# Optimization experiments

Hardware: AMD Instinct MI355X
Metric: run time of the kernel (lower is better)

The kernel has to match this reference:

```python
import jax, jax.numpy as jnp
import numpy as np

N, F_IN, HID, H1, E = 50000, 512, 128, 4, 800000
NEG_SLOPE = 0.2

def setup_inputs() -> dict:
    key = jax.random.key(0)
    ks = jax.random.split(key, 10)
    s = lambda fan: 1.0 / np.sqrt(fan)
    x = jax.random.normal(ks[0], (N, F_IN), jnp.float32)
    edge_index = jax.random.randint(ks[1], (2, E), 0, N, jnp.int32)
    W1 = jax.random.normal(ks[2], (F_IN, H1 * HID), jnp.float32) * s(F_IN)
    a_src1 = jax.random.normal(ks[3], (H1, HID), jnp.float32) * s(HID)
    a_dst1 = jax.random.normal(ks[4], (H1, HID), jnp.float32) * s(HID)
    b1 = jnp.zeros((H1 * HID,), jnp.float32)
    W2 = jax.random.normal(ks[5], (H1 * HID, HID), jnp.float32) * s(H1 * HID)
    a_src2 = jax.random.normal(ks[6], (1, HID), jnp.float32) * s(HID)
    a_dst2 = jax.random.normal(ks[7], (1, HID), jnp.float32) * s(HID)
    b2 = jnp.zeros((HID,), jnp.float32)
    return {"x": x, "edge_index": edge_index, "W1": W1, "a_src1": a_src1,
            "a_dst1": a_dst1, "b1": b1, "W2": W2, "a_src2": a_src2,
            "a_dst2": a_dst2, "b2": b2}

def _gat(x, src, dst, W, a_src, a_dst, b, n):
    H, C = a_src.shape
    h = (x @ W).reshape(-1, H, C)                      # [N, H, C]
    # per-edge attention logits: alpha_src[src] + alpha_dst[dst]
    e = jax.nn.leaky_relu((h * a_src).sum(-1)[src] + (h * a_dst).sum(-1)[dst],
                          NEG_SLOPE)                   # [E', H]
    # segment softmax over destination node
    m = jax.ops.segment_max(e, dst, num_segments=n)
    p = jnp.exp(e - m[dst])
    denom = jax.ops.segment_sum(p, dst, num_segments=n)
    alpha = p / (denom[dst] + 1e-16)
    # weighted scatter-add aggregation
    out = jax.ops.segment_sum(h[src] * alpha[:, :, None], dst, num_segments=n)
    return out.reshape(-1, H * C) + b

def reference(x, edge_index, W1, a_src1, a_dst1, b1, W2, a_src2, a_dst2, b2):
    loops = jnp.arange(N, dtype=edge_index.dtype)      # add_self_loops=True
    src = jnp.concatenate([edge_index[0], loops])
    dst = jnp.concatenate([edge_index[1], loops])
    h = jax.nn.elu(_gat(x, src, dst, W1, a_src1, a_dst1, b1, N))
    return _gat(h, src, dst, W2, a_src2, a_dst2, b2, N)
```

## Files before the change

kernel.cpp:

```cpp
#include <hip/hip_runtime.h>
#include <hip/hip_bf16.h>
#include <math.h>

#define NEG_SLOPE 0.2f

constexpr int N_NODES = 50000;
constexpr int F_IN    = 512;
constexpr int HID     = 128;
constexpr int H1      = 4;
constexpr int E_EDGES = 800000;
constexpr int E_TOT   = E_EDGES + N_NODES;

typedef __attribute__((ext_vector_type(8))) short short8;
typedef __attribute__((ext_vector_type(4))) float floatx4;
typedef __attribute__((ext_vector_type(8))) unsigned short ushort8v;
typedef __attribute__((ext_vector_type(4))) unsigned short ushort4v;
typedef __attribute__((ext_vector_type(2))) unsigned short ushort2v;

__device__ __forceinline__ unsigned short f2bf(float f) {
  union { float f; unsigned int u; } v; v.f = f;
  unsigned int u = v.u + 0x7FFFu + ((v.u >> 16) & 1u);
  return (unsigned short)(u >> 16);
}
__device__ __forceinline__ float bf2f(unsigned short b) {
  union { unsigned int u; float f; } v; v.u = ((unsigned int)b) << 16; return v.f;
}

__device__ __forceinline__ void store_val(float* p, float v) { *p = v; }
__device__ __forceinline__ void store_val(unsigned short* p, float v) { *p = f2bf(v); }

template <int CPT>
__device__ __forceinline__ void load_cvt(const unsigned short* p, float* v) {
  if constexpr (CPT == 8) {
    ushort8v u = *(const ushort8v*)p;
#pragma unroll
    for (int c = 0; c < 8; ++c) v[c] = bf2f(u[c]);
  } else if constexpr (CPT == 4) {
    ushort4v u = *(const ushort4v*)p;
#pragma unroll
    for (int c = 0; c < 4; ++c) v[c] = bf2f(u[c]);
  } else {
    ushort2v u = *(const ushort2v*)p;
#pragma unroll
    for (int c = 0; c < 2; ++c) v[c] = bf2f(u[c]);
  }
}
template <int CPT>
__device__ __forceinline__ void load_cvt(const float* p, float* v) {
#pragma unroll
  for (int c = 0; c < CPT; c += 4) *(float4*)(v + c) = *(const float4*)(p + c);
}

template <int CPT>
__device__ __forceinline__ void store_vec(unsigned short* p, const float* v) {
  if constexpr (CPT == 8) {
    ushort8v o;
#pragma unroll
    for (int c = 0; c < 8; ++c) o[c] = f2bf(v[c]);
    *(ushort8v*)p = o;
  } else if constexpr (CPT == 4) {
    ushort4v o;
#pragma unroll
    for (int c = 0; c < 4; ++c) o[c] = f2bf(v[c]);
    *(ushort4v*)p = o;
  } else {
    ushort2v o;
#pragma unroll
    for (int c = 0; c < 2; ++c) o[c] = f2bf(v[c]);
    *(ushort2v*)p = o;
  }
}
template <int CPT>
__device__ __forceinline__ void store_vec(float* p, const float* v) {
#pragma unroll
  for (int c = 0; c < CPT; c += 4) *(float4*)(p + c) = *(const float4*)(v + c);
}

__device__ __forceinline__ void async_load16(const void* g, void* lds) {
  __builtin_amdgcn_global_load_lds(
      (const __attribute__((address_space(1))) unsigned int*)g,
      (__attribute__((address_space(3))) unsigned int*)lds, 16, 0, 0);
}

__global__ void zero_int_kernel(int* p, int n) {
  int i = blockIdx.x * blockDim.x + threadIdx.x;
  if (i < n) p[i] = 0;
}

__global__ void hist_kernel(const int* __restrict__ ei, int* __restrict__ counts) {
  int i = blockIdx.x * blockDim.x + threadIdx.x;
  if (i < E_EDGES) {
    atomicAdd(&counts[ei[E_EDGES + i]], 1);
  } else if (i < E_TOT) {
    atomicAdd(&counts[i - E_EDGES], 1);
  }
}

__global__ void scan1_kernel(const int* __restrict__ cnt, int* __restrict__ part,
                             int* __restrict__ bsum, int n) {
  __shared__ int buf[256];
  int tid = threadIdx.x, i = blockIdx.x * 256 + tid;
  int v = (i < n) ? cnt[i] : 0;
  buf[tid] = v;
  __syncthreads();
  for (int s = 1; s < 256; s <<= 1) {
    int t = (tid >= s) ? buf[tid - s] : 0;
    __syncthreads();
    buf[tid] += t;
    __syncthreads();
  }
  if (i < n) part[i] = buf[tid] - v;
  if (tid == 255) bsum[blockIdx.x] = buf[255];
}

__global__ void scan2_kernel(int* __restrict__ bsum, int nb) {
  __shared__ int buf[256];
  int tid = threadIdx.x;
  int v = (tid < nb) ? bsum[tid] : 0;
  buf[tid] = v;
  __syncthreads();
  for (int s = 1; s < 256; s <<= 1) {
    int t = (tid >= s) ? buf[tid - s] : 0;
    __syncthreads();
    buf[tid] += t;
    __syncthreads();
  }
  if (tid < nb) bsum[tid] = buf[tid] - v;
  if (tid == 255) bsum[nb] = buf[255];
}

__global__ void scan3_kernel(const int* __restrict__ part, const int* __restrict__ bsum,
                             int* __restrict__ offs, int n) {
  int i = blockIdx.x * 256 + threadIdx.x;
  if (i < n) offs[i] = part[i] + bsum[blockIdx.x];
  if (i == 0) offs[n] = bsum[(n + 255) / 256];
}

__global__ void scatter_kernel(const int* __restrict__ ei, const int* __restrict__ offs,
                               int* __restrict__ cursor, int* __restrict__ sorted_src) {
  int i = blockIdx.x * blockDim.x + threadIdx.x;
  if (i >= E_TOT) return;
  int s, d;
  if (i < E_EDGES) { s = ei[i]; d = ei[E_EDGES + i]; }
  else             { s = i - E_EDGES; d = s; }
  int pos = offs[d] + atomicAdd(&cursor[d], 1);
  sorted_src[pos] = s;
}

__global__ void cast4_kernel(const float* __restrict__ in, unsigned short* __restrict__ out,
                             long n4) {
  long i = (long)blockIdx.x * blockDim.x + threadIdx.x;
  if (i >= n4) return;
  float4 v = ((const float4*)in)[i];
  ushort4 o;
  o.x = f2bf(v.x); o.y = f2bf(v.y); o.z = f2bf(v.z); o.w = f2bf(v.w);
  ((ushort4*)out)[i] = o;
}

__global__ void tcast_kernel(const float* __restrict__ in, unsigned short* __restrict__ out,
                             int K, int N) {
  int idx = blockIdx.x * blockDim.x + threadIdx.x;
  if (idx >= K * N) return;
  int n = idx / K, k = idx - n * K;
  out[idx] = f2bf(in[k * N + n]);
}

template <typename OT>
__global__ __launch_bounds__(256) void gemm_bf16_kernel(
    const unsigned short* __restrict__ A, const unsigned short* __restrict__ Bt,
    OT* __restrict__ C, const float* __restrict__ a_srcp, const float* __restrict__ a_dstp,
    float* __restrict__ alpha_src, float* __restrict__ alpha_dst,
    int M, int N, int K, int Hn) {
  __shared__ unsigned short As[128 * 32];
  __shared__ unsigned short Bs[128 * 32];
  __shared__ float red_s[128][2];
  __shared__ float red_d[128][2];
  int tid = threadIdx.x;
  int lane = tid & 63, wave = tid >> 6;
  int wm = wave & 1, wn = wave >> 1;
  int row0 = blockIdx.x * 128;
  int head = blockIdx.y;
  int col0 = head * 128;
  int l15 = lane & 15, quad = lane >> 4;

  floatx4 acc[4][4];
#pragma unroll
  for (int i = 0; i < 4; ++i)
#pragma unroll
    for (int j = 0; j < 4; ++j) acc[i][j] = (floatx4){0.f, 0.f, 0.f, 0.f};

  int seg_a = wave * 2;
  int r_in = (lane >> 2);
  int c8 = (lane & 3) * 8;

  for (int k0 = 0; k0 < K; k0 += 32) {
#pragma unroll
    for (int p = 0; p < 2; ++p) {
      int seg = seg_a + p;
      int r = seg * 16 + r_in;
      int gr = row0 + r; if (gr >= M) gr = M - 1;
      async_load16(A + (size_t)gr * K + k0 + c8, &As[seg * 512]);
      int gc = col0 + r;
      async_load16(Bt + (size_t)gc * K + k0 + c8, &Bs[seg * 512]);
    }
    __syncthreads();

    short8 a[4], b[4];
#pragma unroll
    for (int mi = 0; mi < 4; ++mi)
      a[mi] = *(const short8*)&As[(wm * 64 + mi * 16 + l15) * 32 + quad * 8];
#pragma unroll
    for (int ni = 0; ni < 4; ++ni)
      b[ni] = *(const short8*)&Bs[(wn * 64 + ni * 16 + l15) * 32 + quad * 8];
#pragma unroll
    for (int mi = 0; mi < 4; ++mi)
#pragma unroll
      for (int ni = 0; ni < 4; ++ni)
        acc[mi][ni] = __builtin_amdgcn_mfma_f32_16x16x32_bf16(a[mi], b[ni], acc[mi][ni], 0, 0, 0);
    __syncthreads();
  }

  float a_s[4], a_d[4];
#pragma unroll
  for (int ni = 0; ni < 4; ++ni) {
    int cih = wn * 64 + ni * 16 + l15;
    a_s[ni] = a_srcp[head * HID + cih];
    a_d[ni] = a_dstp[head * HID + cih];
  }

#pragma unroll
  for (int mi = 0; mi < 4; ++mi) {
#pragma unroll
    for (int r = 0; r < 4; ++r) {
      int rloc = wm * 64 + mi * 16 + quad * 4 + r;
      int grow = row0 + rloc;
      float ps = 0.f, pd = 0.f;
#pragma unroll
      for (int ni = 0; ni < 4; ++ni) {
        float v = acc[mi][ni][r];
        ps += v * a_s[ni];
        pd += v * a_d[ni];
        if (grow < M) {
          int gcol = col0 + wn * 64 + ni * 16 + l15;
          store_val(&C[(size_t)grow * N + gcol], v);
        }
      }
#pragma unroll
      for (int off = 1; off < 16; off <<= 1) {
        ps += __shfl_xor(ps, off);
        pd += __shfl_xor(pd, off);
      }
      if (l15 == 0) { red_s[rloc][wn] = ps; red_d[rloc][wn] = pd; }
    }
  }
  __syncthreads();
  if (tid < 128) {
    int grow = row0 + tid;
    if (grow < M) {
      alpha_src[(size_t)grow * Hn + head] = red_s[tid][0] + red_s[tid][1];
      alpha_dst[(size_t)grow * Hn + head] = red_d[tid][0] + red_d[tid][1];
    }
  }
}

template <int H, int CPT, typename GT, typename OT>
__global__ __launch_bounds__(64) void aggregate_kernel(
    const GT* __restrict__ h, const float* __restrict__ asrc,
    const float* __restrict__ adst, const int* __restrict__ offs,
    const int* __restrict__ sorted_src, const float* __restrict__ bias,
    OT* __restrict__ out, int apply_elu) {
  constexpr int CH = H * HID;
  constexpr int NCH = CH / CPT;
  constexpr int SLOTS = 64 / NCH;
  __shared__ float p_sh[64 * H];
  __shared__ int src_sh[64];
  int node = blockIdx.x;
  int lane = threadIdx.x;
  int off = offs[node];
  int deg = offs[node + 1] - off;
  if (deg > 64) deg = 64;

  int s_i = 0;
  if (lane < deg) s_i = sorted_src[off + lane];
  src_sh[lane] = s_i;

  float ar[H];
#pragma unroll
  for (int hh = 0; hh < H; ++hh) ar[hh] = (lane < deg) ? asrc[s_i * H + hh] : 0.f;
#pragma unroll
  for (int hh = 0; hh < H; ++hh) {
    float v = ar[hh] + adst[node * H + hh];
    v = (v > 0.f) ? v : NEG_SLOPE * v;
    float lg = (lane < deg) ? v : -1e30f;
#pragma unroll
    for (int o = 32; o; o >>= 1) lg = fmaxf(lg, __shfl_xor(lg, o));
    float p = (lane < deg) ? expf(v - lg) : 0.f;
    float s = p;
#pragma unroll
    for (int o = 32; o; o >>= 1) s += __shfl_xor(s, o);
    p_sh[lane * H + hh] = p * (1.f / (s + 1e-16f));
  }
  __syncthreads();

  int chlane = lane % NCH;
  int slot = lane / NCH;
  int ch = chlane * CPT;
  constexpr int HEAD_SHIFT = 7;
  int head = ch >> HEAD_SHIFT;

  float acc[CPT];
#pragma unroll
  for (int c = 0; c < CPT; ++c) acc[c] = 0.f;

  auto body = [&](int e) {
    float w = p_sh[e * H + head];
    const GT* pp = h + (size_t)src_sh[e] * CH + ch;
    float vv[CPT];
    load_cvt<CPT>(pp, vv);
#pragma unroll
    for (int c = 0; c < CPT; ++c) acc[c] += vv[c] * w;
  };
  int e = slot;
  for (; e + 3 * SLOTS < deg; e += 4 * SLOTS) {
    body(e); body(e + SLOTS); body(e + 2 * SLOTS); body(e + 3 * SLOTS);
  }
  for (; e < deg; e += SLOTS) body(e);

  if constexpr (SLOTS == 2) {
#pragma unroll
    for (int c = 0; c < CPT; ++c) acc[c] += __shfl_xor(acc[c], 32);
  }
  if (slot == 0) {
    float r[CPT];
#pragma unroll
    for (int c = 0; c < CPT; ++c) {
      float t = acc[c] + bias[ch + c];
      if (apply_elu) t = (t > 0.f) ? t : (expf(t) - 1.f);
      r[c] = t;
    }
    store_vec<CPT>(&out[(size_t)node * CH + ch], r);
  }
}

extern "C" void kernel_launch(void* const* d_in, const int* in_sizes, int n_in,
                              void* d_out, int out_size, void* d_ws, size_t ws_size,
                              hipStream_t stream) {
  const float* x      = (const float*)d_in[0];
  const int*   ei     = (const int*)d_in[1];
  const float* W1     = (const float*)d_in[2];
  const float* a_src1 = (const float*)d_in[3];
  const float* a_dst1 = (const float*)d_in[4];
  const float* b1     = (const float*)d_in[5];
  const float* W2     = (const float*)d_in[6];
  const float* a_src2 = (const float*)d_in[7];
  const float* a_dst2 = (const float*)d_in[8];
  const float* b2     = (const float*)d_in[9];
  float* out = (float*)d_out;

  float* ws   = (float*)d_ws;
  float* as1  = ws;
  float* ad1  = as1 + N_NODES * H1;
  float* as2  = ad1 + N_NODES * H1;
  float* ad2  = as2 + N_NODES;
  unsigned short* xb    = (unsigned short*)(ad2 + N_NODES);
  unsigned short* h1b   = xb + (size_t)N_NODES * 512;
  unsigned short* hmidb = h1b + (size_t)N_NODES * 512;
  unsigned short* h2b   = hmidb + (size_t)N_NODES * 512;
  unsigned short* W1t   = h2b + (size_t)N_NODES * 128;
  unsigned short* W2t   = W1t + 512 * 512;
  int* counts = (int*)(W2t + 128 * 512);
  int* cursor = counts + N_NODES;
  int* offs   = cursor + N_NODES;
  int* ssrc   = offs + N_NODES + 1;
  int* part   = ssrc + E_TOT;
  int* bsum   = part + N_NODES;

  constexpr int NB = (N_NODES + 255) / 256;

  zero_int_kernel<<<(2 * N_NODES + 255) / 256, 256, 0, stream>>>(counts, 2 * N_NODES);
  hist_kernel<<<(E_TOT + 255) / 256, 256, 0, stream>>>(ei, counts);
  scan1_kernel<<<NB, 256, 0, stream>>>(counts, part, bsum, N_NODES);
  scan2_kernel<<<1, 256, 0, stream>>>(bsum, NB);
  scan3_kernel<<<NB, 256, 0, stream>>>(part, bsum, offs, N_NODES);
  scatter_kernel<<<(E_TOT + 255) / 256, 256, 0, stream>>>(ei, offs, cursor, ssrc);

  long n4x = (long)N_NODES * 512 / 4;
  cast4_kernel<<<(int)((n4x + 255) / 256), 256, 0, stream>>>(x, xb, n4x);
  tcast_kernel<<<(512 * 512 + 255) / 256, 256, 0, stream>>>(W1, W1t, 512, 512);
  tcast_kernel<<<(512 * 128 + 255) / 256, 256, 0, stream>>>(W2, W2t, 512, 128);

  dim3 g1((N_NODES + 127) / 128, 4);
  gemm_bf16_kernel<unsigned short><<<g1, 256, 0, stream>>>(
      xb, W1t, h1b, a_src1, a_dst1, as1, ad1, N_NODES, 512, 512, H1);
  aggregate_kernel<4, 8, unsigned short, unsigned short><<<N_NODES, 64, 0, stream>>>(
      h1b, as1, ad1, offs, ssrc, b1, hmidb, 1);

  dim3 g2((N_NODES + 127) / 128, 1);
  gemm_bf16_kernel<unsigned short><<<g2, 256, 0, stream>>>(
      hmidb, W2t, h2b, a_src2, a_dst2, as2, ad2, N_NODES, 128, 512, 1);
  aggregate_kernel<1, 4, unsigned short, float><<<N_NODES, 64, 0, stream>>>(
      h2b, as2, ad2, offs, ssrc, b2, out, 0);
}
```

Baseline: 515.8 us.

## Pack four nodes per aggregate block and reuse workspace buffers

The aggregate kernel now runs four destination nodes per 256-thread block, one wave each, instead of one 64-thread block per node. This cuts block launch and scheduling overhead and adds a bounds guard for the last partial block. It also precomputes row offsets in shared memory, unrolls the edge loop by eight with a two-wide tail, and aliases the workspace buffers (x cast with hmid, h1 with h2) to shrink the memory footprint. The in-place aliasing depends on stream ordering between the kernels. The added __syncthreads now synchronizes four waves that have different degrees.

```diff
diff --git a/kernel.cpp b/kernel.cpp
--- a/kernel.cpp
+++ b/kernel.cpp
@@ -44,11 +44,6 @@
 #pragma unroll
     for (int c = 0; c < 2; ++c) v[c] = bf2f(u[c]);
   }
-}
-template <int CPT>
-__device__ __forceinline__ void load_cvt(const float* p, float* v) {
-#pragma unroll
-  for (int c = 0; c < CPT; c += 4) *(float4*)(v + c) = *(const float4*)(p + c);
 }
 
 template <int CPT>
@@ -264,7 +259,7 @@
 }
 
 template <int H, int CPT, typename GT, typename OT>
-__global__ __launch_bounds__(64) void aggregate_kernel(
+__global__ __launch_bounds__(256) void aggregate_kernel(
     const GT* __restrict__ h, const float* __restrict__ asrc,
     const float* __restrict__ adst, const int* __restrict__ offs,
     const int* __restrict__ sorted_src, const float* __restrict__ bias,
@@ -272,24 +267,26 @@
   constexpr int CH = H * HID;
   constexpr int NCH = CH / CPT;
   constexpr int SLOTS = 64 / NCH;
-  __shared__ float p_sh[64 * H];
-  __shared__ int src_sh[64];
-  int node = blockIdx.x;
-  int lane = threadIdx.x;
-  int off = offs[node];
-  int deg = offs[node + 1] - off;
+  __shared__ float p_sh[4][64 * H];
+  __shared__ int rowoff_sh[4][64];
+  int lane = threadIdx.x & 63;
+  int wave = threadIdx.x >> 6;
+  int node = blockIdx.x * 4 + wave;
+  bool live = node < N_NODES;
+  int off = live ? offs[node] : 0;
+  int deg = live ? (offs[node + 1] - off) : 0;
   if (deg > 64) deg = 64;
 
   int s_i = 0;
   if (lane < deg) s_i = sorted_src[off + lane];
-  src_sh[lane] = s_i;
+  rowoff_sh[wave][lane] = s_i * CH;
 
   float ar[H];
 #pragma unroll
   for (int hh = 0; hh < H; ++hh) ar[hh] = (lane < deg) ? asrc[s_i * H + hh] : 0.f;
 #pragma unroll
   for (int hh = 0; hh < H; ++hh) {
-    float v = ar[hh] + adst[node * H + hh];
+    float v = live ? (ar[hh] + adst[node * H + hh]) : 0.f;
     v = (v > 0.f) ? v : NEG_SLOPE * v;
     float lg = (lane < deg) ? v : -1e30f;
 #pragma unroll
@@ -298,39 +295,42 @@
     float s = p;
 #pragma unroll
     for (int o = 32; o; o >>= 1) s += __shfl_xor(s, o);
-    p_sh[lane * H + hh] = p * (1.f / (s + 1e-16f));
+    p_sh[wave][lane * H + hh] = p * (1.f / (s + 1e-16f));
   }
   __syncthreads();
 
   int chlane = lane % NCH;
   int slot = lane / NCH;
   int ch = chlane * CPT;
-  constexpr int HEAD_SHIFT = 7;
-  int head = ch >> HEAD_SHIFT;
+  int head = ch >> 7;
 
   float acc[CPT];
 #pragma unroll
   for (int c = 0; c < CPT; ++c) acc[c] = 0.f;
 
+  const float* pw = &p_sh[wave][0];
+  const int* ro = &rowoff_sh[wave][0];
   auto body = [&](int e) {
-    float w = p_sh[e * H + head];
-    const GT* pp = h + (size_t)src_sh[e] * CH + ch;
+    float w = pw[e * H + head];
+    const GT* pp = h + (size_t)(unsigned)ro[e] + ch;
     float vv[CPT];
     load_cvt<CPT>(pp, vv);
 #pragma unroll
     for (int c = 0; c < CPT; ++c) acc[c] += vv[c] * w;
   };
   int e = slot;
-  for (; e + 3 * SLOTS < deg; e += 4 * SLOTS) {
+  for (; e + 7 * SLOTS < deg; e += 8 * SLOTS) {
     body(e); body(e + SLOTS); body(e + 2 * SLOTS); body(e + 3 * SLOTS);
-  }
+    body(e + 4 * SLOTS); body(e + 5 * SLOTS); body(e + 6 * SLOTS); body(e + 7 * SLOTS);
+  }
+  for (; e + SLOTS < deg; e += 2 * SLOTS) { body(e); body(e + SLOTS); }
   for (; e < deg; e += SLOTS) body(e);
 
-  if constexpr (SLOTS == 2) {
+  if constexpr (SLOTS >= 2) {
 #pragma unroll
     for (int c = 0; c < CPT; ++c) acc[c] += __shfl_xor(acc[c], 32);
   }
-  if (slot == 0) {
+  if (live && slot == 0) {
     float r[CPT];
 #pragma unroll
     for (int c = 0; c < CPT; ++c) {
@@ -362,11 +362,13 @@
   float* ad1  = as1 + N_NODES * H1;
   float* as2  = ad1 + N_NODES * H1;
   float* ad2  = as2 + N_NODES;
-  unsigned short* xb    = (unsigned short*)(ad2 + N_NODES);
-  unsigned short* h1b   = xb + (size_t)N_NODES * 512;
-  unsigned short* hmidb = h1b + (size_t)N_NODES * 512;
-  unsigned short* h2b   = hmidb + (size_t)N_NODES * 512;
-  unsigned short* W1t   = h2b + (size_t)N_NODES * 128;
+  unsigned short* bufA = (unsigned short*)(ad2 + N_NODES);
+  unsigned short* bufB = bufA + (size_t)N_NODES * 512;
+  unsigned short* xb    = bufA;
+  unsigned short* hmidb = bufA;
+  unsigned short* h1b   = bufB;
+  unsigned short* h2b   = bufB;
+  unsigned short* W1t   = bufB + (size_t)N_NODES * 512;
   unsigned short* W2t   = W1t + 512 * 512;
   int* counts = (int*)(W2t + 128 * 512);
   int* cursor = counts + N_NODES;
@@ -392,12 +394,14 @@
   dim3 g1((N_NODES + 127) / 128, 4);
   gemm_bf16_kernel<unsigned short><<<g1, 256, 0, stream>>>(
       xb, W1t, h1b, a_src1, a_dst1, as1, ad1, N_NODES, 512, 512, H1);
-  aggregate_kernel<4, 8, unsigned short, unsigned short><<<N_NODES, 64, 0, stream>>>(
+  aggregate_kernel<4, 8, unsigned short, unsigned short>
+      <<<(N_NODES + 3) / 4, 256, 0, stream>>>(
       h1b, as1, ad1, offs, ssrc, b1, hmidb, 1);
 
   dim3 g2((N_NODES + 127) / 128, 1);
   gemm_bf16_kernel<unsigned short><<<g2, 256, 0, stream>>>(
       hmidb, W2t, h2b, a_src2, a_dst2, as2, ad2, N_NODES, 128, 512, 1);
-  aggregate_kernel<1, 4, unsigned short, float><<<N_NODES, 64, 0, stream>>>(
+  aggregate_kernel<1, 4, unsigned short, float>
+      <<<(N_NODES + 3) / 4, 256, 0, stream>>>(
       h2b, as2, ad2, offs, ssrc, b2, out, 0);
 }
```

After: 518.8 us. Within noise of the previous version (+0.6%).
